# Optimization experiments

Hardware: AMD Instinct MI355X
Metric: run time of the kernel (lower is better)

Reference implementation:

```python
import jax, jax.numpy as jnp
import numpy as np

B, S, E, H = 2, 2048, 1024, 16
D = E // H


def setup_inputs() -> dict:
    key = jax.random.key(0)
    ks = jax.random.split(key, 11)
    def lin(k):
        kw, kb = jax.random.split(k)
        bound = 1.0 / np.sqrt(E)
        W = jax.random.uniform(kw, (E, E), jnp.float32, -bound, bound)
        b = jax.random.uniform(kb, (E,), jnp.float32, -bound, bound)
        return W, b
    Wq, bq = lin(ks[0])
    Wk, bk = lin(ks[1])
    Wv, bv = lin(ks[2])
    Wo, bo = lin(ks[3])
    return {
        "query": jax.random.normal(ks[4], (B, S, E), jnp.float32),
        "key": jax.random.normal(ks[5], (B, S, E), jnp.float32),
        "value": jax.random.normal(ks[6], (B, S, E), jnp.float32),
        "Wq": Wq, "bq": bq, "Wk": Wk, "bk": bk,
        "Wv": Wv, "bv": bv, "Wo": Wo, "bo": bo,
        "is_causal": 1,
    }


def reference(query, key, value, Wq, bq, Wk, bk, Wv, bv, Wo, bo, is_causal):
    scale = D ** -0.5
    def heads(x, W, b):
        # torch Linear: x @ W.T + b, then [B,S,H,D] -> [B,H,S,D]
        y = jnp.einsum('bse,fe->bsf', x, W) + b
        return y.reshape(B, S, H, D).transpose(0, 2, 1, 3)
    q = heads(query, Wq, bq)
    k = heads(key, Wk, bk)
    v = heads(value, Wv, bv)
    scores = jnp.einsum('bhqd,bhkd->bhqk', q, k) * scale  # [B,H,S,S]
    if is_causal:
        mask = jnp.tril(jnp.ones((S, S), dtype=bool))
        scores = jnp.where(mask, scores, -jnp.inf)
    attn = jax.nn.softmax(scores, axis=-1)
    out = jnp.einsum('bhqk,bhkd->bhqd', attn, v)
    out = out.transpose(0, 2, 1, 3).reshape(B, S, E)
    return jnp.einsum('bse,fe->bsf', out, Wo) + bo
```

## Files before the change

### kernel.cpp

```cpp
#include <hip/hip_runtime.h>
#include <cstdint>
#include <cstddef>

typedef unsigned short u16;
typedef unsigned int u32;
typedef __attribute__((ext_vector_type(8))) short bf16x8;
typedef __attribute__((ext_vector_type(4))) float f32x4;
typedef __attribute__((ext_vector_type(16))) float f32x16;
typedef __attribute__((ext_vector_type(4))) u16 u16x4;
typedef __attribute__((ext_vector_type(4))) u32 u32x4;
typedef __attribute__((ext_vector_type(2))) u32 u32x2;

__device__ __forceinline__ u16 f2bf(float f) {
  u32 x = __builtin_bit_cast(u32, f);
  x += 0x7fffu + ((x >> 16) & 1u);
  return (u16)(x >> 16);
}

__device__ __forceinline__ void g2lds16(const u16* g, u16* l) {
  __builtin_amdgcn_global_load_lds(
      (const __attribute__((address_space(1))) u32*)g,
      (__attribute__((address_space(3))) u32*)l, 16, 0, 0);
}

struct CvtArgs { const float* s[7]; u16* d[7]; int n4[7]; };

__global__ __launch_bounds__(256) void cvt_all(CvtArgs a) {
  int y = blockIdx.y;
  const float4* __restrict__ src = (const float4*)a.s[y];
  u16* __restrict__ dst = a.d[y];
  int n4 = a.n4[y];
  for (int i = blockIdx.x * blockDim.x + threadIdx.x; i < n4;
       i += gridDim.x * blockDim.x) {
    float4 v = src[i];
    u16x4 o = { f2bf(v.x), f2bf(v.y), f2bf(v.z), f2bf(v.w) };
    *(u16x4*)(dst + (size_t)i * 4) = o;
  }
}

struct GemmArgs {
  const u16* A[3]; const u16* W[3]; const float* bias[3];
  void* out[3]; float scale[3]; int mode[3];
};

__global__ __launch_bounds__(256) void gemm_fused(GemmArgs ga) {
  __shared__ alignas(16) u16 As[2][128 * 32];
  __shared__ alignas(16) u16 Bs[2][128 * 32];
  const int z = blockIdx.z;
  const u16* __restrict__ A = ga.A[z];
  const u16* __restrict__ W = ga.W[z];
  const int tid = threadIdx.x;
  const int lane = tid & 63;
  const int w = tid >> 6;
  const int lo4 = lane & 15, hi2 = lane >> 4;
  const int l = (int)blockIdx.x + 8 * (int)blockIdx.y;
  const int wl = (l & 7) * 32 + (l >> 3);
  const int m0 = (wl >> 3) * 128;
  const int n0 = (wl & 7) * 128;
  const int wr = w >> 1, wc = w & 1;

  f32x4 acc[4][4] = {};

  auto stage = [&](int kt, int buf) {
    const int k0 = kt * 32;
#pragma unroll
    for (int i = 0; i < 2; ++i) {
      int c = (i * 4 + w) * 64 + lane;
      int r = c >> 2;
      int q = (c & 3) ^ ((r >> 1) & 3);
      g2lds16(A + (size_t)(m0 + r) * 1024 + k0 + q * 8, As[buf] + (i * 4 + w) * 512);
      g2lds16(W + (size_t)(n0 + r) * 1024 + k0 + q * 8, Bs[buf] + (i * 4 + w) * 512);
    }
  };

  stage(0, 0);
  __syncthreads();
  int cur = 0;
  for (int kt = 0; kt < 32; ++kt) {
    if (kt + 1 < 32) stage(kt + 1, cur ^ 1);
    bf16x8 af[4], bfr[4];
#pragma unroll
    for (int i = 0; i < 4; ++i) {
      int r = wr * 64 + i * 16 + lo4;
      int q = hi2 ^ ((r >> 1) & 3);
      af[i] = *(const bf16x8*)(As[cur] + r * 32 + q * 8);
    }
#pragma unroll
    for (int j = 0; j < 4; ++j) {
      int r = wc * 64 + j * 16 + lo4;
      int q = hi2 ^ ((r >> 1) & 3);
      bfr[j] = *(const bf16x8*)(Bs[cur] + r * 32 + q * 8);
    }
#pragma unroll
    for (int i = 0; i < 4; ++i)
#pragma unroll
      for (int j = 0; j < 4; ++j)
        acc[i][j] = __builtin_amdgcn_mfma_f32_16x16x32_bf16(af[i], bfr[j], acc[i][j], 0, 0, 0);
    __syncthreads();
    cur ^= 1;
  }

  const float* __restrict__ bias = ga.bias[z];
  const float cs = ga.scale[z];
  const int mode = ga.mode[z];
#pragma unroll
  for (int j = 0; j < 4; ++j) {
    int n = n0 + wc * 64 + j * 16 + lo4;
    float bv = bias[n];
#pragma unroll
    for (int i = 0; i < 4; ++i) {
#pragma unroll
      for (int rg = 0; rg < 4; ++rg) {
        int m = m0 + wr * 64 + i * 16 + hi2 * 4 + rg;
        float v = (acc[i][j][rg] + bv) * cs;
        if (mode == 2) {
          ((float*)ga.out[z])[(size_t)m * 1024 + n] = v;
        } else {
          int b = m >> 11, s = m & 2047, h = n >> 6, d = n & 63;
          size_t addr = (mode == 0)
            ? ((size_t)(b * 16 + h) * 2048 + s) * 64 + d
            : ((size_t)(b * 16 + h) * 64 + d) * 2048 + s;
          ((u16*)ga.out[z])[addr] = f2bf(v);
        }
      }
    }
  }
}

__global__ __launch_bounds__(512) void attn_kernel(
    const u16* __restrict__ Q, const u16* __restrict__ K,
    const u16* __restrict__ Vt, u16* __restrict__ Out,
    const int* __restrict__ causal_p) {
  __shared__ alignas(16) u16 Ks[2][2][64 * 64];
  __shared__ alignas(16) u16 Vs[2][2][64 * 64];
  const int tid = threadIdx.x, lane = tid & 63, w = tid >> 6;
  const int wg = w >> 2, wi = w & 3;
  const int ql = lane & 31, hi = lane >> 5;
  const int bh = blockIdx.y;
  const int qt = (bh < 16) ? (int)blockIdx.x : 15 - (int)blockIdx.x;
  const int causal = *causal_p;
  const u16* Qb = Q + (size_t)bh * 2048 * 64;
  const u16* Kb = K + (size_t)bh * 2048 * 64;
  const u16* Vb = Vt + (size_t)bh * 64 * 2048;

  const int q0b = qt * 128 + wi * 32;
  const int qrow = q0b + ql;

  bf16x8 qf[4];
#pragma unroll
  for (int dsl = 0; dsl < 4; ++dsl)
    qf[dsl] = *(const bf16x8*)(Qb + (size_t)qrow * 64 + dsl * 16 + hi * 8);

  auto stageKV = [&](int jt, int buf) {
#pragma unroll
    for (int i = 0; i < 2; ++i) {
      int c = (i * 4 + wi) * 64 + lane;
      int r = c >> 3;
      int q = (c & 7) ^ (r & 7);
      g2lds16(Kb + (size_t)(jt * 64 + r) * 64 + q * 8, Ks[wg][buf] + (i * 4 + wi) * 512);
      g2lds16(Vb + (size_t)r * 2048 + jt * 64 + q * 8, Vs[wg][buf] + (i * 4 + wi) * 512);
    }
  };

  const int nt_w = causal ? (2 * qt + 1 + (wi >> 1)) : 32;
  const int U = causal ? (qt + 1) : 16;

  stageKV(wg, 0);
  __syncthreads();

  float m_r = -1e30f, l_r = 0.f;
  f32x16 o0 = {}, o1 = {};
  int cur = 0;

  for (int u = 0; u < U; ++u) {
    const int jt = 2 * u + wg;
    if (u + 1 < U) stageKV(jt + 2, cur ^ 1);

    if (jt < nt_w) {
      f32x16 s0 = {}, s1 = {};
#pragma unroll
      for (int dsl = 0; dsl < 4; ++dsl) {
        int cc = dsl * 2 + hi;
        bf16x8 k0 = *(const bf16x8*)(Ks[wg][cur] + ql * 64 + ((cc ^ (ql & 7)) * 8));
        bf16x8 k1 = *(const bf16x8*)(Ks[wg][cur] + (32 + ql) * 64 + ((cc ^ (ql & 7)) * 8));
        s0 = __builtin_amdgcn_mfma_f32_32x32x16_bf16(k0, qf[dsl], s0, 0, 0, 0);
        s1 = __builtin_amdgcn_mfma_f32_32x32x16_bf16(k1, qf[dsl], s1, 0, 0, 0);
      }

      if (causal && jt == nt_w - 1) {
#pragma unroll
        for (int rg = 0; rg < 16; ++rg) {
          int kof = jt * 64 + 8 * (rg >> 2) + (rg & 3) + 4 * hi;
          s0[rg] = (kof > qrow) ? -1e30f : s0[rg];
          s1[rg] = (kof + 32 > qrow) ? -1e30f : s1[rg];
        }
      }

      float pm = fmaxf(s0[0], s1[0]);
#pragma unroll
      for (int rg = 1; rg < 16; ++rg) pm = fmaxf(pm, fmaxf(s0[rg], s1[rg]));
      pm = fmaxf(pm, __shfl_xor(pm, 32));
      if (!__all(pm <= m_r + 8.f)) {
        float mn = fmaxf(m_r, pm);
        float corr = exp2f(m_r - mn);
        m_r = mn;
        l_r *= corr;
#pragma unroll
        for (int rg = 0; rg < 16; ++rg) { o0[rg] *= corr; o1[rg] *= corr; }
      }
      float sum = 0.f;
#pragma unroll
      for (int rg = 0; rg < 16; ++rg) { s0[rg] = exp2f(s0[rg] - m_r); sum += s0[rg]; }
#pragma unroll
      for (int rg = 0; rg < 16; ++rg) { s1[rg] = exp2f(s1[rg] - m_r); sum += s1[rg]; }
      sum += __shfl_xor(sum, 32);
      l_r += sum;

#pragma unroll
      for (int s = 0; s < 4; ++s) {
        const f32x16& p = (s >= 2) ? s1 : s0;
        const int base = 8 * (s & 1);
        u32 A0, A1, B0, B1;
        asm("v_cvt_pk_bf16_f32 %0, %1, %2" : "=v"(A0) : "v"(p[base + 0]), "v"(p[base + 1]));
        asm("v_cvt_pk_bf16_f32 %0, %1, %2" : "=v"(A1) : "v"(p[base + 2]), "v"(p[base + 3]));
        asm("v_cvt_pk_bf16_f32 %0, %1, %2" : "=v"(B0) : "v"(p[base + 4]), "v"(p[base + 5]));
        asm("v_cvt_pk_bf16_f32 %0, %1, %2" : "=v"(B1) : "v"(p[base + 6]), "v"(p[base + 7]));
        asm volatile("v_permlane32_swap_b32 %0, %1" : "+v"(A0), "+v"(B0));
        asm volatile("v_permlane32_swap_b32 %0, %1" : "+v"(A1), "+v"(B1));
        u32x4 pw = {A0, A1, B0, B1};
        bf16x8 pf = __builtin_bit_cast(bf16x8, pw);
#pragma unroll
        for (int df = 0; df < 2; ++df) {
          int rr = df * 32 + ql;
          bf16x8 vf = *(const bf16x8*)(Vs[wg][cur] + rr * 64 + (((s * 2 + hi) ^ (rr & 7)) * 8));
          if (df) o1 = __builtin_amdgcn_mfma_f32_32x32x16_bf16(vf, pf, o1, 0, 0, 0);
          else    o0 = __builtin_amdgcn_mfma_f32_32x32x16_bf16(vf, pf, o0, 0, 0, 0);
        }
      }
    }
    __syncthreads();
    cur ^= 1;
  }

  float* Od = (float*)&Ks[0][0][0];
  float* ml = (float*)&Vs[0][0][0];
  __syncthreads();
  if (wg == 1) {
#pragma unroll
    for (int rg = 0; rg < 16; ++rg) {
      Od[rg * 256 + wi * 64 + lane] = o0[rg];
      Od[(16 + rg) * 256 + wi * 64 + lane] = o1[rg];
    }
    ml[wi * 64 + lane] = m_r;
    ml[256 + wi * 64 + lane] = l_r;
  }
  __syncthreads();
  if (wg == 0) {
    float m_b = ml[wi * 64 + lane];
    float l_b = ml[256 + wi * 64 + lane];
    float mn = fmaxf(m_r, m_b);
    float ca = exp2f(m_r - mn), cb = exp2f(m_b - mn);
    float rl = 1.f / (l_r * ca + l_b * cb);
    const int batch = bh >> 4, h = bh & 15;
    u16* orow = Out + ((size_t)(batch * 2048 + qrow)) * 1024 + h * 64;
#pragma unroll
    for (int df = 0; df < 2; ++df) {
      const f32x16& oo = df ? o1 : o0;
#pragma unroll
      for (int b2 = 0; b2 < 4; ++b2) {
        u32 w0, w1;
        float v0, v1, v2, v3;
        v0 = (oo[4 * b2 + 0] * ca + Od[(df * 16 + 4 * b2 + 0) * 256 + wi * 64 + lane] * cb) * rl;
        v1 = (oo[4 * b2 + 1] * ca + Od[(df * 16 + 4 * b2 + 1) * 256 + wi * 64 + lane] * cb) * rl;
        v2 = (oo[4 * b2 + 2] * ca + Od[(df * 16 + 4 * b2 + 2) * 256 + wi * 64 + lane] * cb) * rl;
        v3 = (oo[4 * b2 + 3] * ca + Od[(df * 16 + 4 * b2 + 3) * 256 + wi * 64 + lane] * cb) * rl;
        asm("v_cvt_pk_bf16_f32 %0, %1, %2" : "=v"(w0) : "v"(v0), "v"(v1));
        asm("v_cvt_pk_bf16_f32 %0, %1, %2" : "=v"(w1) : "v"(v2), "v"(v3));
        int d0 = df * 32 + b2 * 8 + hi * 4;
        u32x2 pr = {w0, w1};
        *(u32x2*)(orow + d0) = pr;
      }
    }
  }
}

extern "C" void kernel_launch(void* const* d_in, const int* in_sizes, int n_in,
                              void* d_out, int out_size, void* d_ws, size_t ws_size,
                              hipStream_t stream) {
  (void)in_sizes; (void)n_in; (void)out_size; (void)ws_size;
  const float* query = (const float*)d_in[0];
  const float* key   = (const float*)d_in[1];
  const float* value = (const float*)d_in[2];
  const float* Wq = (const float*)d_in[3];
  const float* bq = (const float*)d_in[4];
  const float* Wk = (const float*)d_in[5];
  const float* bk = (const float*)d_in[6];
  const float* Wv = (const float*)d_in[7];
  const float* bv = (const float*)d_in[8];
  const float* Wo = (const float*)d_in[9];
  const float* bo = (const float*)d_in[10];
  const int* is_causal = (const int*)d_in[11];

  u16* wsp = (u16*)d_ws;
  u16* xq  = wsp;
  u16* xk  = xq  + (4u << 20);
  u16* xv  = xk  + (4u << 20);
  u16* wq  = xv  + (4u << 20);
  u16* wk  = wq  + (1u << 20);
  u16* wv  = wk  + (1u << 20);
  u16* wo  = wv  + (1u << 20);
  u16* Qb  = wo  + (1u << 20);
  u16* Kb  = Qb  + (4u << 20);
  u16* Vtb = Kb  + (4u << 20);
  u16* attn= Vtb + (4u << 20);

  CvtArgs ca;
  ca.s[0] = query; ca.d[0] = xq; ca.n4[0] = 1 << 20;
  ca.s[1] = key;   ca.d[1] = xk; ca.n4[1] = 1 << 20;
  ca.s[2] = value; ca.d[2] = xv; ca.n4[2] = 1 << 20;
  ca.s[3] = Wq; ca.d[3] = wq; ca.n4[3] = 1 << 18;
  ca.s[4] = Wk; ca.d[4] = wk; ca.n4[4] = 1 << 18;
  ca.s[5] = Wv; ca.d[5] = wv; ca.n4[5] = 1 << 18;
  ca.s[6] = Wo; ca.d[6] = wo; ca.n4[6] = 1 << 18;
  cvt_all<<<dim3(512, 7), 256, 0, stream>>>(ca);

  const float LOG2E = 1.4426950408889634f;
  GemmArgs g1;
  g1.A[0] = xq; g1.W[0] = wq; g1.bias[0] = bq; g1.out[0] = Qb;
  g1.scale[0] = 0.125f * LOG2E; g1.mode[0] = 0;
  g1.A[1] = xk; g1.W[1] = wk; g1.bias[1] = bk; g1.out[1] = Kb;
  g1.scale[1] = 1.f; g1.mode[1] = 0;
  g1.A[2] = xv; g1.W[2] = wv; g1.bias[2] = bv; g1.out[2] = Vtb;
  g1.scale[2] = 1.f; g1.mode[2] = 1;
  gemm_fused<<<dim3(8, 32, 3), 256, 0, stream>>>(g1);

  attn_kernel<<<dim3(16, 32), 512, 0, stream>>>(Qb, Kb, Vtb, attn, is_causal);

  GemmArgs g2;
  for (int i = 0; i < 3; ++i) {
    g2.A[i] = attn; g2.W[i] = wo; g2.bias[i] = bo; g2.out[i] = d_out;
    g2.scale[i] = 1.f; g2.mode[i] = 2;
  }
  gemm_fused<<<dim3(8, 32, 1), 256, 0, stream>>>(g2);
}
```

Measured before the change: 150.3 us.

## Give each attention wave two 32-row query tiles to reuse K/V fragments

The attention block shrinks from 8 waves to 4. Each wave now processes 64 query rows as two 32-row sub-tiles, so every K and V fragment read from LDS feeds two MFMAs instead of one. This halves LDS read traffic per FLOP and lets independent MFMA chains interleave. The cost is roughly double the accumulator and score registers, which lowers occupancy (launch bounds 256,2), plus a different LDS layout for the cross-wave merge. The syncthreads before the merge was dropped.

```diff
diff --git a/kernel.cpp b/kernel.cpp
--- a/kernel.cpp
+++ b/kernel.cpp
@@ -127,14 +127,14 @@
   }
 }
 
-__global__ __launch_bounds__(512) void attn_kernel(
+__global__ __launch_bounds__(256, 2) void attn_kernel(
     const u16* __restrict__ Q, const u16* __restrict__ K,
     const u16* __restrict__ Vt, u16* __restrict__ Out,
     const int* __restrict__ causal_p) {
   __shared__ alignas(16) u16 Ks[2][2][64 * 64];
   __shared__ alignas(16) u16 Vs[2][2][64 * 64];
   const int tid = threadIdx.x, lane = tid & 63, w = tid >> 6;
-  const int wg = w >> 2, wi = w & 3;
+  const int wg = w >> 1, wv = w & 1;
   const int ql = lane & 31, hi = lane >> 5;
   const int bh = blockIdx.y;
   const int qt = (bh < 16) ? (int)blockIdx.x : 15 - (int)blockIdx.x;
@@ -143,98 +143,123 @@
   const u16* Kb = K + (size_t)bh * 2048 * 64;
   const u16* Vb = Vt + (size_t)bh * 64 * 2048;
 
-  const int q0b = qt * 128 + wi * 32;
-  const int qrow = q0b + ql;
-
-  bf16x8 qf[4];
-#pragma unroll
-  for (int dsl = 0; dsl < 4; ++dsl)
-    qf[dsl] = *(const bf16x8*)(Qb + (size_t)qrow * 64 + dsl * 16 + hi * 8);
+  const int qA = qt * 128 + wv * 64 + ql;
+  const int qB = qA + 32;
+
+  bf16x8 qfA[4], qfB[4];
+#pragma unroll
+  for (int dsl = 0; dsl < 4; ++dsl) {
+    qfA[dsl] = *(const bf16x8*)(Qb + (size_t)qA * 64 + dsl * 16 + hi * 8);
+    qfB[dsl] = *(const bf16x8*)(Qb + (size_t)qB * 64 + dsl * 16 + hi * 8);
+  }
 
   auto stageKV = [&](int jt, int buf) {
 #pragma unroll
-    for (int i = 0; i < 2; ++i) {
-      int c = (i * 4 + wi) * 64 + lane;
+    for (int i = 0; i < 4; ++i) {
+      int c = i * 128 + wv * 64 + lane;
       int r = c >> 3;
       int q = (c & 7) ^ (r & 7);
-      g2lds16(Kb + (size_t)(jt * 64 + r) * 64 + q * 8, Ks[wg][buf] + (i * 4 + wi) * 512);
-      g2lds16(Vb + (size_t)r * 2048 + jt * 64 + q * 8, Vs[wg][buf] + (i * 4 + wi) * 512);
+      g2lds16(Kb + (size_t)(jt * 64 + r) * 64 + q * 8, Ks[wg][buf] + (i * 128 + wv * 64) * 8);
+      g2lds16(Vb + (size_t)r * 2048 + jt * 64 + q * 8, Vs[wg][buf] + (i * 128 + wv * 64) * 8);
     }
   };
 
-  const int nt_w = causal ? (2 * qt + 1 + (wi >> 1)) : 32;
+  const int nt_w = causal ? (2 * qt + wv + 1) : 32;
   const int U = causal ? (qt + 1) : 16;
 
   stageKV(wg, 0);
   __syncthreads();
 
-  float m_r = -1e30f, l_r = 0.f;
-  f32x16 o0 = {}, o1 = {};
+  float mA = -1e30f, lA = 0.f, mB = -1e30f, lB = 0.f;
+  f32x16 oA0 = {}, oA1 = {}, oB0 = {}, oB1 = {};
   int cur = 0;
+
+  auto online_sm = [&](f32x16& s0, f32x16& s1, float& m_r, float& l_r,
+                       f32x16& o0, f32x16& o1) {
+    float pm = fmaxf(s0[0], s1[0]);
+#pragma unroll
+    for (int rg = 1; rg < 16; ++rg) pm = fmaxf(pm, fmaxf(s0[rg], s1[rg]));
+    pm = fmaxf(pm, __shfl_xor(pm, 32));
+    if (!__all(pm <= m_r + 8.f)) {
+      float mn = fmaxf(m_r, pm);
+      float corr = exp2f(m_r - mn);
+      m_r = mn; l_r *= corr;
+#pragma unroll
+      for (int rg = 0; rg < 16; ++rg) { o0[rg] *= corr; o1[rg] *= corr; }
+    }
+    float sum = 0.f;
+#pragma unroll
+    for (int rg = 0; rg < 16; ++rg) { s0[rg] = exp2f(s0[rg] - m_r); sum += s0[rg]; }
+#pragma unroll
+    for (int rg = 0; rg < 16; ++rg) { s1[rg] = exp2f(s1[rg] - m_r); sum += s1[rg]; }
+    sum += __shfl_xor(sum, 32);
+    l_r += sum;
+  };
 
   for (int u = 0; u < U; ++u) {
     const int jt = 2 * u + wg;
     if (u + 1 < U) stageKV(jt + 2, cur ^ 1);
 
     if (jt < nt_w) {
-      f32x16 s0 = {}, s1 = {};
+      f32x16 sA0 = {}, sA1 = {}, sB0 = {}, sB1 = {};
 #pragma unroll
       for (int dsl = 0; dsl < 4; ++dsl) {
         int cc = dsl * 2 + hi;
         bf16x8 k0 = *(const bf16x8*)(Ks[wg][cur] + ql * 64 + ((cc ^ (ql & 7)) * 8));
         bf16x8 k1 = *(const bf16x8*)(Ks[wg][cur] + (32 + ql) * 64 + ((cc ^ (ql & 7)) * 8));
-        s0 = __builtin_amdgcn_mfma_f32_32x32x16_bf16(k0, qf[dsl], s0, 0, 0, 0);
-        s1 = __builtin_amdgcn_mfma_f32_32x32x16_bf16(k1, qf[dsl], s1, 0, 0, 0);
+        sA0 = __builtin_amdgcn_mfma_f32_32x32x16_bf16(k0, qfA[dsl], sA0, 0, 0, 0);
+        sB0 = __builtin_amdgcn_mfma_f32_32x32x16_bf16(k0, qfB[dsl], sB0, 0, 0, 0);
+        sA1 = __builtin_amdgcn_mfma_f32_32x32x16_bf16(k1, qfA[dsl], sA1, 0, 0, 0);
+        sB1 = __builtin_amdgcn_mfma_f32_32x32x16_bf16(k1, qfB[dsl], sB1, 0, 0, 0);
       }
 
       if (causal && jt == nt_w - 1) {
 #pragma unroll
         for (int rg = 0; rg < 16; ++rg) {
           int kof = jt * 64 + 8 * (rg >> 2) + (rg & 3) + 4 * hi;
-          s0[rg] = (kof > qrow) ? -1e30f : s0[rg];
-          s1[rg] = (kof + 32 > qrow) ? -1e30f : s1[rg];
+          sA0[rg] = (kof > qA) ? -1e30f : sA0[rg];
+          sA1[rg] = (kof + 32 > qA) ? -1e30f : sA1[rg];
+          sB0[rg] = (kof > qB) ? -1e30f : sB0[rg];
+          sB1[rg] = (kof + 32 > qB) ? -1e30f : sB1[rg];
         }
       }
 
-      float pm = fmaxf(s0[0], s1[0]);
-#pragma unroll
-      for (int rg = 1; rg < 16; ++rg) pm = fmaxf(pm, fmaxf(s0[rg], s1[rg]));
-      pm = fmaxf(pm, __shfl_xor(pm, 32));
-      if (!__all(pm <= m_r + 8.f)) {
-        float mn = fmaxf(m_r, pm);
-        float corr = exp2f(m_r - mn);
-        m_r = mn;
-        l_r *= corr;
-#pragma unroll
-        for (int rg = 0; rg < 16; ++rg) { o0[rg] *= corr; o1[rg] *= corr; }
-      }
-      float sum = 0.f;
-#pragma unroll
-      for (int rg = 0; rg < 16; ++rg) { s0[rg] = exp2f(s0[rg] - m_r); sum += s0[rg]; }
-#pragma unroll
-      for (int rg = 0; rg < 16; ++rg) { s1[rg] = exp2f(s1[rg] - m_r); sum += s1[rg]; }
-      sum += __shfl_xor(sum, 32);
-      l_r += sum;
+      online_sm(sA0, sA1, mA, lA, oA0, oA1);
+      online_sm(sB0, sB1, mB, lB, oB0, oB1);
 
 #pragma unroll
       for (int s = 0; s < 4; ++s) {
-        const f32x16& p = (s >= 2) ? s1 : s0;
+        const f32x16& pA = (s >= 2) ? sA1 : sA0;
+        const f32x16& pB = (s >= 2) ? sB1 : sB0;
         const int base = 8 * (s & 1);
-        u32 A0, A1, B0, B1;
-        asm("v_cvt_pk_bf16_f32 %0, %1, %2" : "=v"(A0) : "v"(p[base + 0]), "v"(p[base + 1]));
-        asm("v_cvt_pk_bf16_f32 %0, %1, %2" : "=v"(A1) : "v"(p[base + 2]), "v"(p[base + 3]));
-        asm("v_cvt_pk_bf16_f32 %0, %1, %2" : "=v"(B0) : "v"(p[base + 4]), "v"(p[base + 5]));
-        asm("v_cvt_pk_bf16_f32 %0, %1, %2" : "=v"(B1) : "v"(p[base + 6]), "v"(p[base + 7]));
-        asm volatile("v_permlane32_swap_b32 %0, %1" : "+v"(A0), "+v"(B0));
-        asm volatile("v_permlane32_swap_b32 %0, %1" : "+v"(A1), "+v"(B1));
-        u32x4 pw = {A0, A1, B0, B1};
-        bf16x8 pf = __builtin_bit_cast(bf16x8, pw);
+        u32 a0, a1, b0, b1, c0, c1, d0_, d1;
+        asm("v_cvt_pk_bf16_f32 %0, %1, %2" : "=v"(a0) : "v"(pA[base + 0]), "v"(pA[base + 1]));
+        asm("v_cvt_pk_bf16_f32 %0, %1, %2" : "=v"(a1) : "v"(pA[base + 2]), "v"(pA[base + 3]));
+        asm("v_cvt_pk_bf16_f32 %0, %1, %2" : "=v"(b0) : "v"(pA[base + 4]), "v"(pA[base + 5]));
+        asm("v_cvt_pk_bf16_f32 %0, %1, %2" : "=v"(b1) : "v"(pA[base + 6]), "v"(pA[base + 7]));
+        asm volatile("v_permlane32_swap_b32 %0, %1" : "+v"(a0), "+v"(b0));
+        asm volatile("v_permlane32_swap_b32 %0, %1" : "+v"(a1), "+v"(b1));
+        asm("v_cvt_pk_bf16_f32 %0, %1, %2" : "=v"(c0) : "v"(pB[base + 0]), "v"(pB[base + 1]));
+        asm("v_cvt_pk_bf16_f32 %0, %1, %2" : "=v"(c1) : "v"(pB[base + 2]), "v"(pB[base + 3]));
+        asm("v_cvt_pk_bf16_f32 %0, %1, %2" : "=v"(d0_) : "v"(pB[base + 4]), "v"(pB[base + 5]));
+        asm("v_cvt_pk_bf16_f32 %0, %1, %2" : "=v"(d1) : "v"(pB[base + 6]), "v"(pB[base + 7]));
+        asm volatile("v_permlane32_swap_b32 %0, %1" : "+v"(c0), "+v"(d0_));
+        asm volatile("v_permlane32_swap_b32 %0, %1" : "+v"(c1), "+v"(d1));
+        u32x4 pwA = {a0, a1, b0, b1};
+        u32x4 pwB = {c0, c1, d0_, d1};
+        bf16x8 pfA = __builtin_bit_cast(bf16x8, pwA);
+        bf16x8 pfB = __builtin_bit_cast(bf16x8, pwB);
 #pragma unroll
         for (int df = 0; df < 2; ++df) {
           int rr = df * 32 + ql;
           bf16x8 vf = *(const bf16x8*)(Vs[wg][cur] + rr * 64 + (((s * 2 + hi) ^ (rr & 7)) * 8));
-          if (df) o1 = __builtin_amdgcn_mfma_f32_32x32x16_bf16(vf, pf, o1, 0, 0, 0);
-          else    o0 = __builtin_amdgcn_mfma_f32_32x32x16_bf16(vf, pf, o0, 0, 0, 0);
+          if (df) {
+            oA1 = __builtin_amdgcn_mfma_f32_32x32x16_bf16(vf, pfA, oA1, 0, 0, 0);
+            oB1 = __builtin_amdgcn_mfma_f32_32x32x16_bf16(vf, pfB, oB1, 0, 0, 0);
+          } else {
+            oA0 = __builtin_amdgcn_mfma_f32_32x32x16_bf16(vf, pfA, oA0, 0, 0, 0);
+            oB0 = __builtin_amdgcn_mfma_f32_32x32x16_bf16(vf, pfB, oB0, 0, 0, 0);
+          }
         }
       }
     }
@@ -244,41 +269,49 @@
 
   float* Od = (float*)&Ks[0][0][0];
   float* ml = (float*)&Vs[0][0][0];
-  __syncthreads();
+  const int li = wv * 64 + lane;
   if (wg == 1) {
 #pragma unroll
     for (int rg = 0; rg < 16; ++rg) {
-      Od[rg * 256 + wi * 64 + lane] = o0[rg];
-      Od[(16 + rg) * 256 + wi * 64 + lane] = o1[rg];
-    }
-    ml[wi * 64 + lane] = m_r;
-    ml[256 + wi * 64 + lane] = l_r;
+      Od[((li * 2 + 0) * 2 + 0) * 16 + rg] = oA0[rg];
+      Od[((li * 2 + 0) * 2 + 1) * 16 + rg] = oA1[rg];
+      Od[((li * 2 + 1) * 2 + 0) * 16 + rg] = oB0[rg];
+      Od[((li * 2 + 1) * 2 + 1) * 16 + rg] = oB1[rg];
+    }
+    ml[li * 4 + 0] = mA; ml[li * 4 + 1] = lA;
+    ml[li * 4 + 2] = mB; ml[li * 4 + 3] = lB;
   }
   __syncthreads();
   if (wg == 0) {
-    float m_b = ml[wi * 64 + lane];
-    float l_b = ml[256 + wi * 64 + lane];
-    float mn = fmaxf(m_r, m_b);
-    float ca = exp2f(m_r - mn), cb = exp2f(m_b - mn);
-    float rl = 1.f / (l_r * ca + l_b * cb);
     const int batch = bh >> 4, h = bh & 15;
-    u16* orow = Out + ((size_t)(batch * 2048 + qrow)) * 1024 + h * 64;
-#pragma unroll
-    for (int df = 0; df < 2; ++df) {
-      const f32x16& oo = df ? o1 : o0;
-#pragma unroll
-      for (int b2 = 0; b2 < 4; ++b2) {
-        u32 w0, w1;
-        float v0, v1, v2, v3;
-        v0 = (oo[4 * b2 + 0] * ca + Od[(df * 16 + 4 * b2 + 0) * 256 + wi * 64 + lane] * cb) * rl;
-        v1 = (oo[4 * b2 + 1] * ca + Od[(df * 16 + 4 * b2 + 1) * 256 + wi * 64 + lane] * cb) * rl;
-        v2 = (oo[4 * b2 + 2] * ca + Od[(df * 16 + 4 * b2 + 2) * 256 + wi * 64 + lane] * cb) * rl;
-        v3 = (oo[4 * b2 + 3] * ca + Od[(df * 16 + 4 * b2 + 3) * 256 + wi * 64 + lane] * cb) * rl;
-        asm("v_cvt_pk_bf16_f32 %0, %1, %2" : "=v"(w0) : "v"(v0), "v"(v1));
-        asm("v_cvt_pk_bf16_f32 %0, %1, %2" : "=v"(w1) : "v"(v2), "v"(v3));
-        int d0 = df * 32 + b2 * 8 + hi * 4;
-        u32x2 pr = {w0, w1};
-        *(u32x2*)(orow + d0) = pr;
+#pragma unroll
+    for (int sub = 0; sub < 2; ++sub) {
+      float m_r = sub ? mB : mA;
+      float l_r = sub ? lB : lA;
+      float m_b = ml[li * 4 + sub * 2 + 0];
+      float l_b = ml[li * 4 + sub * 2 + 1];
+      float mn = fmaxf(m_r, m_b);
+      float ca = exp2f(m_r - mn), cb = exp2f(m_b - mn);
+      float rl = 1.f / (l_r * ca + l_b * cb);
+      int qrow = sub ? qB : qA;
+      u16* orow = Out + ((size_t)(batch * 2048 + qrow)) * 1024 + h * 64;
+#pragma unroll
+      for (int df = 0; df < 2; ++df) {
+        const f32x16& oo = sub ? (df ? oB1 : oB0) : (df ? oA1 : oA0);
+        const float* Op = &Od[((li * 2 + sub) * 2 + df) * 16];
+#pragma unroll
+        for (int b2 = 0; b2 < 4; ++b2) {
+          u32 w0, w1;
+          float v0 = (oo[4 * b2 + 0] * ca + Op[4 * b2 + 0] * cb) * rl;
+          float v1 = (oo[4 * b2 + 1] * ca + Op[4 * b2 + 1] * cb) * rl;
+          float v2 = (oo[4 * b2 + 2] * ca + Op[4 * b2 + 2] * cb) * rl;
+          float v3 = (oo[4 * b2 + 3] * ca + Op[4 * b2 + 3] * cb) * rl;
+          asm("v_cvt_pk_bf16_f32 %0, %1, %2" : "=v"(w0) : "v"(v0), "v"(v1));
+          asm("v_cvt_pk_bf16_f32 %0, %1, %2" : "=v"(w1) : "v"(v2), "v"(v3));
+          int d0 = df * 32 + b2 * 8 + hi * 4;
+          u32x2 pr = {w0, w1};
+          *(u32x2*)(orow + d0) = pr;
+        }
       }
     }
   }
@@ -334,7 +367,7 @@
   g1.scale[2] = 1.f; g1.mode[2] = 1;
   gemm_fused<<<dim3(8, 32, 3), 256, 0, stream>>>(g1);
 
-  attn_kernel<<<dim3(16, 32), 512, 0, stream>>>(Qb, Kb, Vtb, attn, is_causal);
+  attn_kernel<<<dim3(16, 32), 256, 0, stream>>>(Qb, Kb, Vtb, attn, is_causal);
 
   GemmArgs g2;
   for (int i = 0; i < 3; ++i) {
```

Result: faster. 142.9 us (-4.9%).

## Deepen prefetch pipelines and restructure attention into paired causal q-tiles

Applied to the files above, without the earlier changes.

The GEMM now prefetches two k-tiles ahead, synchronising with explicit vmcnt waits and raw barriers instead of a full __syncthreads per iteration. The attention kernel moves to 256-thread blocks (2 per CU) that each process a light and a heavy causal 64-row q-tile pair (slot and 31-slot) to balance work. It also remaps block indices to heads, uses a two-deep KV prefetch with vmcnt-based waits, and lays out the LDS merge buffer per lane. These changes aim to hide global-load latency and even out causal load imbalance, at the cost of more fragile manual wait-count accounting.

```diff
diff --git a/kernel.cpp b/kernel.cpp
--- a/kernel.cpp
+++ b/kernel.cpp
@@ -74,10 +74,11 @@
   };
 
   stage(0, 0);
-  __syncthreads();
-  int cur = 0;
+  stage(1, 1);
   for (int kt = 0; kt < 32; ++kt) {
-    if (kt + 1 < 32) stage(kt + 1, cur ^ 1);
+    const int cur = kt & 1;
+    asm volatile("s_waitcnt vmcnt(4)" ::: "memory");
+    __builtin_amdgcn_s_barrier();
     bf16x8 af[4], bfr[4];
 #pragma unroll
     for (int i = 0; i < 4; ++i) {
@@ -96,9 +97,10 @@
 #pragma unroll
       for (int j = 0; j < 4; ++j)
         acc[i][j] = __builtin_amdgcn_mfma_f32_16x16x32_bf16(af[i], bfr[j], acc[i][j], 0, 0, 0);
-    __syncthreads();
-    cur ^= 1;
-  }
+    __builtin_amdgcn_s_barrier();
+    stage(kt + 2 < 32 ? kt + 2 : kt, cur);
+  }
+  asm volatile("s_waitcnt vmcnt(0)" ::: "memory");
 
   const float* __restrict__ bias = ga.bias[z];
   const float cs = ga.scale[z];
@@ -127,160 +129,167 @@
   }
 }
 
-__global__ __launch_bounds__(512) void attn_kernel(
+__global__ __launch_bounds__(256, 2) void attn_kernel(
     const u16* __restrict__ Q, const u16* __restrict__ K,
     const u16* __restrict__ Vt, u16* __restrict__ Out,
     const int* __restrict__ causal_p) {
   __shared__ alignas(16) u16 Ks[2][2][64 * 64];
   __shared__ alignas(16) u16 Vs[2][2][64 * 64];
+  __shared__ float ml2[256];
   const int tid = threadIdx.x, lane = tid & 63, w = tid >> 6;
-  const int wg = w >> 2, wi = w & 3;
+  const int wg = w >> 1, wv = w & 1;
   const int ql = lane & 31, hi = lane >> 5;
-  const int bh = blockIdx.y;
-  const int qt = (bh < 16) ? (int)blockIdx.x : 15 - (int)blockIdx.x;
+  const int bx = (int)blockIdx.x, by = (int)blockIdx.y;
+  const int bh = (bx & 7) * 4 + (by >> 3);
+  const int slot = ((bx >> 3) << 3) | (by & 7);
   const int causal = *causal_p;
   const u16* Qb = Q + (size_t)bh * 2048 * 64;
   const u16* Kb = K + (size_t)bh * 2048 * 64;
   const u16* Vb = Vt + (size_t)bh * 64 * 2048;
-
-  const int q0b = qt * 128 + wi * 32;
-  const int qrow = q0b + ql;
-
-  bf16x8 qf[4];
-#pragma unroll
-  for (int dsl = 0; dsl < 4; ++dsl)
-    qf[dsl] = *(const bf16x8*)(Qb + (size_t)qrow * 64 + dsl * 16 + hi * 8);
+  const int batch = bh >> 4, h = bh & 15;
 
   auto stageKV = [&](int jt, int buf) {
 #pragma unroll
-    for (int i = 0; i < 2; ++i) {
-      int c = (i * 4 + wi) * 64 + lane;
+    for (int i = 0; i < 4; ++i) {
+      int c = i * 128 + wv * 64 + lane;
       int r = c >> 3;
       int q = (c & 7) ^ (r & 7);
-      g2lds16(Kb + (size_t)(jt * 64 + r) * 64 + q * 8, Ks[wg][buf] + (i * 4 + wi) * 512);
-      g2lds16(Vb + (size_t)r * 2048 + jt * 64 + q * 8, Vs[wg][buf] + (i * 4 + wi) * 512);
+      g2lds16(Kb + (size_t)(jt * 64 + r) * 64 + q * 8, Ks[wg][buf] + (i * 128 + wv * 64) * 8);
+      g2lds16(Vb + (size_t)r * 2048 + jt * 64 + q * 8, Vs[wg][buf] + (i * 128 + wv * 64) * 8);
     }
   };
 
-  const int nt_w = causal ? (2 * qt + 1 + (wi >> 1)) : 32;
-  const int U = causal ? (qt + 1) : 16;
-
-  stageKV(wg, 0);
-  __syncthreads();
-
-  float m_r = -1e30f, l_r = 0.f;
-  f32x16 o0 = {}, o1 = {};
-  int cur = 0;
-
-  for (int u = 0; u < U; ++u) {
-    const int jt = 2 * u + wg;
-    if (u + 1 < U) stageKV(jt + 2, cur ^ 1);
-
-    if (jt < nt_w) {
-      f32x16 s0 = {}, s1 = {};
-#pragma unroll
-      for (int dsl = 0; dsl < 4; ++dsl) {
-        int cc = dsl * 2 + hi;
-        bf16x8 k0 = *(const bf16x8*)(Ks[wg][cur] + ql * 64 + ((cc ^ (ql & 7)) * 8));
-        bf16x8 k1 = *(const bf16x8*)(Ks[wg][cur] + (32 + ql) * 64 + ((cc ^ (ql & 7)) * 8));
-        s0 = __builtin_amdgcn_mfma_f32_32x32x16_bf16(k0, qf[dsl], s0, 0, 0, 0);
-        s1 = __builtin_amdgcn_mfma_f32_32x32x16_bf16(k1, qf[dsl], s1, 0, 0, 0);
+  float* Od = (float*)&Ks[0][0][0];
+  const int li = wv * 64 + lane;
+
+  for (int seg = 0; seg < 2; ++seg) {
+    const int qt = seg ? 31 - slot : slot;
+    const int qrow = qt * 64 + wv * 32 + ql;
+
+    bf16x8 qf[4];
+#pragma unroll
+    for (int dsl = 0; dsl < 4; ++dsl)
+      qf[dsl] = *(const bf16x8*)(Qb + (size_t)qrow * 64 + dsl * 16 + hi * 8);
+
+    const int nt = causal ? (qt + 1) : 32;
+    const int U = (nt + 1) >> 1;
+
+    stageKV(wg, 0);
+    stageKV(wg + 2, 1);
+
+    float m_r = -1e30f, l_r = 0.f;
+    f32x16 o0 = {}, o1 = {};
+
+    for (int u = 0; u < U; ++u) {
+      const int jt = 2 * u + wg;
+      const int cur = u & 1;
+      asm volatile("s_waitcnt vmcnt(8)" ::: "memory");
+      __builtin_amdgcn_s_barrier();
+
+      if (jt < nt) {
+        f32x16 s0 = {}, s1 = {};
+#pragma unroll
+        for (int dsl = 0; dsl < 4; ++dsl) {
+          int cc = dsl * 2 + hi;
+          bf16x8 k0 = *(const bf16x8*)(Ks[wg][cur] + ql * 64 + ((cc ^ (ql & 7)) * 8));
+          bf16x8 k1 = *(const bf16x8*)(Ks[wg][cur] + (32 + ql) * 64 + ((cc ^ (ql & 7)) * 8));
+          s0 = __builtin_amdgcn_mfma_f32_32x32x16_bf16(k0, qf[dsl], s0, 0, 0, 0);
+          s1 = __builtin_amdgcn_mfma_f32_32x32x16_bf16(k1, qf[dsl], s1, 0, 0, 0);
+        }
+
+        if (causal && jt == qt) {
+#pragma unroll
+          for (int rg = 0; rg < 16; ++rg) {
+            int kof = jt * 64 + 8 * (rg >> 2) + (rg & 3) + 4 * hi;
+            s0[rg] = (kof > qrow) ? -1e30f : s0[rg];
+            s1[rg] = (kof + 32 > qrow) ? -1e30f : s1[rg];
+          }
+        }
+
+        float pm = fmaxf(s0[0], s1[0]);
+#pragma unroll
+        for (int rg = 1; rg < 16; ++rg) pm = fmaxf(pm, fmaxf(s0[rg], s1[rg]));
+        pm = fmaxf(pm, __shfl_xor(pm, 32));
+        if (!__all(pm <= m_r + 8.f)) {
+          float mn = fmaxf(m_r, pm);
+          float corr = exp2f(m_r - mn);
+          m_r = mn; l_r *= corr;
+#pragma unroll
+          for (int rg = 0; rg < 16; ++rg) { o0[rg] *= corr; o1[rg] *= corr; }
+        }
+        float sum = 0.f;
+#pragma unroll
+        for (int rg = 0; rg < 16; ++rg) { s0[rg] = exp2f(s0[rg] - m_r); sum += s0[rg]; }
+#pragma unroll
+        for (int rg = 0; rg < 16; ++rg) { s1[rg] = exp2f(s1[rg] - m_r); sum += s1[rg]; }
+        sum += __shfl_xor(sum, 32);
+        l_r += sum;
+
+#pragma unroll
+        for (int s = 0; s < 4; ++s) {
+          const f32x16& p = (s >= 2) ? s1 : s0;
+          const int base = 8 * (s & 1);
+          u32 A0, A1, B0, B1;
+          asm("v_cvt_pk_bf16_f32 %0, %1, %2" : "=v"(A0) : "v"(p[base + 0]), "v"(p[base + 1]));
+          asm("v_cvt_pk_bf16_f32 %0, %1, %2" : "=v"(A1) : "v"(p[base + 2]), "v"(p[base + 3]));
+          asm("v_cvt_pk_bf16_f32 %0, %1, %2" : "=v"(B0) : "v"(p[base + 4]), "v"(p[base + 5]));
+          asm("v_cvt_pk_bf16_f32 %0, %1, %2" : "=v"(B1) : "v"(p[base + 6]), "v"(p[base + 7]));
+          asm volatile("v_permlane32_swap_b32 %0, %1" : "+v"(A0), "+v"(B0));
+          asm volatile("v_permlane32_swap_b32 %0, %1" : "+v"(A1), "+v"(B1));
+          u32x4 pw = {A0, A1, B0, B1};
+          bf16x8 pf = __builtin_bit_cast(bf16x8, pw);
+#pragma unroll
+          for (int df = 0; df < 2; ++df) {
+            int rr = df * 32 + ql;
+            bf16x8 vf = *(const bf16x8*)(Vs[wg][cur] + rr * 64 + (((s * 2 + hi) ^ (rr & 7)) * 8));
+            if (df) o1 = __builtin_amdgcn_mfma_f32_32x32x16_bf16(vf, pf, o1, 0, 0, 0);
+            else    o0 = __builtin_amdgcn_mfma_f32_32x32x16_bf16(vf, pf, o0, 0, 0, 0);
+          }
+        }
       }
-
-      if (causal && jt == nt_w - 1) {
-#pragma unroll
-        for (int rg = 0; rg < 16; ++rg) {
-          int kof = jt * 64 + 8 * (rg >> 2) + (rg & 3) + 4 * hi;
-          s0[rg] = (kof > qrow) ? -1e30f : s0[rg];
-          s1[rg] = (kof + 32 > qrow) ? -1e30f : s1[rg];
-        }
+      __builtin_amdgcn_s_barrier();
+      stageKV(u + 2 < U ? jt + 4 : jt, cur);
+    }
+    asm volatile("s_waitcnt vmcnt(0)" ::: "memory");
+    __syncthreads();
+
+    if (wg == 1) {
+#pragma unroll
+      for (int rg = 0; rg < 16; ++rg) {
+        Od[li * 32 + rg]      = o0[rg];
+        Od[li * 32 + 16 + rg] = o1[rg];
       }
-
-      float pm = fmaxf(s0[0], s1[0]);
-#pragma unroll
-      for (int rg = 1; rg < 16; ++rg) pm = fmaxf(pm, fmaxf(s0[rg], s1[rg]));
-      pm = fmaxf(pm, __shfl_xor(pm, 32));
-      if (!__all(pm <= m_r + 8.f)) {
-        float mn = fmaxf(m_r, pm);
-        float corr = exp2f(m_r - mn);
-        m_r = mn;
-        l_r *= corr;
-#pragma unroll
-        for (int rg = 0; rg < 16; ++rg) { o0[rg] *= corr; o1[rg] *= corr; }
+      ml2[li * 2 + 0] = m_r;
+      ml2[li * 2 + 1] = l_r;
+    }
+    __syncthreads();
+    if (wg == 0) {
+      float m_b = ml2[li * 2 + 0];
+      float l_b = ml2[li * 2 + 1];
+      float mn = fmaxf(m_r, m_b);
+      float ca = exp2f(m_r - mn), cb = exp2f(m_b - mn);
+      float rl = 1.f / (l_r * ca + l_b * cb);
+      u16* orow = Out + ((size_t)(batch * 2048 + qrow)) * 1024 + h * 64;
+#pragma unroll
+      for (int df = 0; df < 2; ++df) {
+        const f32x16& oo = df ? o1 : o0;
+        const float* Op = &Od[li * 32 + df * 16];
+#pragma unroll
+        for (int b2 = 0; b2 < 4; ++b2) {
+          u32 w0, w1;
+          float v0 = (oo[4 * b2 + 0] * ca + Op[4 * b2 + 0] * cb) * rl;
+          float v1 = (oo[4 * b2 + 1] * ca + Op[4 * b2 + 1] * cb) * rl;
+          float v2 = (oo[4 * b2 + 2] * ca + Op[4 * b2 + 2] * cb) * rl;
+          float v3 = (oo[4 * b2 + 3] * ca + Op[4 * b2 + 3] * cb) * rl;
+          asm("v_cvt_pk_bf16_f32 %0, %1, %2" : "=v"(w0) : "v"(v0), "v"(v1));
+          asm("v_cvt_pk_bf16_f32 %0, %1, %2" : "=v"(w1) : "v"(v2), "v"(v3));
+          int d0 = df * 32 + b2 * 8 + hi * 4;
+          u32x2 pr = {w0, w1};
+          *(u32x2*)(orow + d0) = pr;
+        }
       }
-      float sum = 0.f;
-#pragma unroll
-      for (int rg = 0; rg < 16; ++rg) { s0[rg] = exp2f(s0[rg] - m_r); sum += s0[rg]; }
-#pragma unroll
-      for (int rg = 0; rg < 16; ++rg) { s1[rg] = exp2f(s1[rg] - m_r); sum += s1[rg]; }
-      sum += __shfl_xor(sum, 32);
-      l_r += sum;
-
-#pragma unroll
-      for (int s = 0; s < 4; ++s) {
-        const f32x16& p = (s >= 2) ? s1 : s0;
-        const int base = 8 * (s & 1);
-        u32 A0, A1, B0, B1;
-        asm("v_cvt_pk_bf16_f32 %0, %1, %2" : "=v"(A0) : "v"(p[base + 0]), "v"(p[base + 1]));
-        asm("v_cvt_pk_bf16_f32 %0, %1, %2" : "=v"(A1) : "v"(p[base + 2]), "v"(p[base + 3]));
-        asm("v_cvt_pk_bf16_f32 %0, %1, %2" : "=v"(B0) : "v"(p[base + 4]), "v"(p[base + 5]));
-        asm("v_cvt_pk_bf16_f32 %0, %1, %2" : "=v"(B1) : "v"(p[base + 6]), "v"(p[base + 7]));
-        asm volatile("v_permlane32_swap_b32 %0, %1" : "+v"(A0), "+v"(B0));
-        asm volatile("v_permlane32_swap_b32 %0, %1" : "+v"(A1), "+v"(B1));
-        u32x4 pw = {A0, A1, B0, B1};
-        bf16x8 pf = __builtin_bit_cast(bf16x8, pw);
-#pragma unroll
-        for (int df = 0; df < 2; ++df) {
-          int rr = df * 32 + ql;
-          bf16x8 vf = *(const bf16x8*)(Vs[wg][cur] + rr * 64 + (((s * 2 + hi) ^ (rr & 7)) * 8));
-          if (df) o1 = __builtin_amdgcn_mfma_f32_32x32x16_bf16(vf, pf, o1, 0, 0, 0);
-          else    o0 = __builtin_amdgcn_mfma_f32_32x32x16_bf16(vf, pf, o0, 0, 0, 0);
-        }
-      }
     }
     __syncthreads();
-    cur ^= 1;
-  }
-
-  float* Od = (float*)&Ks[0][0][0];
-  float* ml = (float*)&Vs[0][0][0];
-  __syncthreads();
-  if (wg == 1) {
-#pragma unroll
-    for (int rg = 0; rg < 16; ++rg) {
-      Od[rg * 256 + wi * 64 + lane] = o0[rg];
-      Od[(16 + rg) * 256 + wi * 64 + lane] = o1[rg];
-    }
-    ml[wi * 64 + lane] = m_r;
-    ml[256 + wi * 64 + lane] = l_r;
-  }
-  __syncthreads();
-  if (wg == 0) {
-    float m_b = ml[wi * 64 + lane];
-    float l_b = ml[256 + wi * 64 + lane];
-    float mn = fmaxf(m_r, m_b);
-    float ca = exp2f(m_r - mn), cb = exp2f(m_b - mn);
-    float rl = 1.f / (l_r * ca + l_b * cb);
-    const int batch = bh >> 4, h = bh & 15;
-    u16* orow = Out + ((size_t)(batch * 2048 + qrow)) * 1024 + h * 64;
-#pragma unroll
-    for (int df = 0; df < 2; ++df) {
-      const f32x16& oo = df ? o1 : o0;
-#pragma unroll
-      for (int b2 = 0; b2 < 4; ++b2) {
-        u32 w0, w1;
-        float v0, v1, v2, v3;
-        v0 = (oo[4 * b2 + 0] * ca + Od[(df * 16 + 4 * b2 + 0) * 256 + wi * 64 + lane] * cb) * rl;
-        v1 = (oo[4 * b2 + 1] * ca + Od[(df * 16 + 4 * b2 + 1) * 256 + wi * 64 + lane] * cb) * rl;
-        v2 = (oo[4 * b2 + 2] * ca + Od[(df * 16 + 4 * b2 + 2) * 256 + wi * 64 + lane] * cb) * rl;
-        v3 = (oo[4 * b2 + 3] * ca + Od[(df * 16 + 4 * b2 + 3) * 256 + wi * 64 + lane] * cb) * rl;
-        asm("v_cvt_pk_bf16_f32 %0, %1, %2" : "=v"(w0) : "v"(v0), "v"(v1));
-        asm("v_cvt_pk_bf16_f32 %0, %1, %2" : "=v"(w1) : "v"(v2), "v"(v3));
-        int d0 = df * 32 + b2 * 8 + hi * 4;
-        u32x2 pr = {w0, w1};
-        *(u32x2*)(orow + d0) = pr;
-      }
-    }
   }
 }
 
@@ -334,7 +343,7 @@
   g1.scale[2] = 1.f; g1.mode[2] = 1;
   gemm_fused<<<dim3(8, 32, 3), 256, 0, stream>>>(g1);
 
-  attn_kernel<<<dim3(16, 32), 512, 0, stream>>>(Qb, Kb, Vtb, attn, is_causal);
+  attn_kernel<<<dim3(16, 32), 256, 0, stream>>>(Qb, Kb, Vtb, attn, is_causal);
 
   GemmArgs g2;
   for (int i = 0; i < 3; ++i) {
```

Result: faster. 128.8 us (-14.3%).
